# Kernel optimization log

Measured on AMD Instinct MI355X. Metric: run time of the kernel, lower is better.

## Reference

```python
import jax, jax.numpy as jnp
import numpy as np

EPS = 1e-8


def setup_inputs() -> dict:
    key = jax.random.key(0)
    k1, k2 = jax.random.split(key)
    N, D = 2048, 1024
    source = jax.random.normal(k1, (N, D), dtype=jnp.float32)
    target = jax.random.normal(k2, (N, D), dtype=jnp.float32)
    return {"source": source, "target": target}


def reference(source, target):
    N = source.shape[0]
    total = jnp.concatenate([source, target], axis=0)          # [2N, D]
    # Pairwise squared L2 via Gram trick: ||a||^2 + ||b||^2 - 2 a.b
    sq = jnp.sum(total * total, axis=-1)                       # [2N]
    gram = total @ total.T                                     # [2N, 2N]
    L2 = jnp.maximum(sq[:, None] + sq[None, :] - 2.0 * gram, 0.0)
    # torch.median on even-length flat array returns the LOWER of the two
    # middle elements, i.e. sorted[(numel - 1) // 2]
    flat = jnp.sort(L2.ravel())
    median_l2 = flat[(flat.size - 1) // 2]
    log_n = jnp.log(jnp.float32(N) + EPS)
    bandwidth = jax.lax.stop_gradient(jnp.sqrt(0.5 * median_l2 / log_n))
    kernel = jnp.exp(-L2 / (2.0 * bandwidth ** 2))             # [2N, 2N]
    XX = kernel[:N, :N]
    YY = kernel[N:, N:]
    XY = kernel[:N, N:]
    YX = kernel[N:, :N]
    loss = jnp.mean(XX + YY - XY - YX)
    return loss, bandwidth
```

## Files before the change

### kernel.cpp

```cpp
#include <hip/hip_runtime.h>

typedef unsigned int uint;
typedef unsigned short ushort;
using short8 = __attribute__((ext_vector_type(8))) short;
using f32x4  = __attribute__((ext_vector_type(4))) float;

#define NHALF 2048
#define DIM   1024
#define MROWS 4096
#define KMED  8388607u
#define NTRI  528

#define AH_OFF   0ull
#define SQ_OFF   8388608ull
#define GHT_OFF  (SQ_OFF + 16384ull)
#define GHN_OFF  (GHT_OFF + 65600ull)
#define CNT_OFF  (GHN_OFF + 65600ull)
#define ZERO_WORDS 32804

#define AGLOAD(p) __hip_atomic_load((p), __ATOMIC_RELAXED, __HIP_MEMORY_SCOPE_AGENT)

__device__ __forceinline__ ushort f2bf(float x) {
    uint u = __float_as_uint(x);
    u += 0x7FFFu + ((u >> 16) & 1u);
    return (ushort)(u >> 16);
}

__global__ __launch_bounds__(256) void convert_kernel(const float* __restrict__ src,
                                                      const float* __restrict__ tgt,
                                                      char* __restrict__ wsb) {
    ushort* ah = (ushort*)(wsb + AH_OFF);
    float*  sq = (float*)(wsb + SQ_OFF);
    uint*   z  = (uint*)(wsb + GHT_OFF);
    int t = threadIdx.x, row = blockIdx.x;
    int g = row * 256 + t;
    if (g < ZERO_WORDS) z[g] = 0;
    const float* p = (row < NHALF) ? src + (size_t)row * DIM
                                   : tgt + (size_t)(row - NHALF) * DIM;
    float4 v = reinterpret_cast<const float4*>(p)[t];
    float xs[4] = {v.x, v.y, v.z, v.w};
    ushort hh[4];
    float s = 0.0f;
#pragma unroll
    for (int e = 0; e < 4; ++e) { float x = xs[e]; s += x * x; hh[e] = f2bf(x); }
    ushort4 h4; h4.x = hh[0]; h4.y = hh[1]; h4.z = hh[2]; h4.w = hh[3];
    reinterpret_cast<ushort4*>(ah + (size_t)row * DIM)[t] = h4;
    for (int o = 32; o; o >>= 1) s += __shfl_down(s, o);
    __shared__ float red[4];
    if ((t & 63) == 0) red[t >> 6] = s;
    __syncthreads();
    if (t == 0) sq[row] = red[0] + red[1] + red[2] + red[3];
}

#define STAGE1(buf, arr, srcp, rb, cidx) do {                                              \
    int _i = (cidx) * 64 + lane;                                                           \
    const ushort* _g = (srcp) + ((size_t)((rb) + (_i >> 2)) * DIM + kk0 + (_i & 3) * 8);   \
    __builtin_amdgcn_global_load_lds(                                                      \
        (const __attribute__((address_space(1))) uint*)_g,                                 \
        (__attribute__((address_space(3))) uint*)(&lds[buf][arr][0][0] + (size_t)(cidx) * 512), \
        16, 0, 0);                                                                         \
} while (0)

__global__ __launch_bounds__(512, 4) void gemm_kernel(char* __restrict__ wsb,
                                                      float* __restrict__ out) {
    const ushort* ah = (const ushort*)(wsb + AH_OFF);
    const float*  sq = (const float*)(wsb + SQ_OFF);
    uint*  ght = (uint*)(wsb + GHT_OFF);
    uint*  ghn = (uint*)(wsb + GHN_OFF);
    uint*  cnt = (uint*)(wsb + CNT_OFF);

    __shared__ __align__(16) uint shmem[8192];
    __shared__ uint lowcnt;
    __shared__ float fred[8];
    ushort (*lds)[2][128][32] = (ushort (*)[2][128][32])shmem;

    int b = (int)blockIdx.x;
    b = (b & 7) * 66 + (b >> 3);
    int bi = (int)((sqrtf(8.0f * (float)b + 1.0f) - 1.0f) * 0.5f);
    while ((bi + 1) * (bi + 2) / 2 <= b) ++bi;
    while (bi * (bi + 1) / 2 > b) --bi;
    int bj = b - bi * (bi + 1) / 2;

    int t = threadIdx.x;
    int lane = t & 63, wid = t >> 6;
    int wm = wid >> 2, wn = wid & 3;
    int rowbase = bi * 128, colbase = bj * 128;

    f32x4 acc[4][2] = {};
    int fr = lane & 15, fk = (lane >> 4) * 8;

    {
        int kk0 = 0;
        STAGE1(0, 0, ah, rowbase, wid);
        STAGE1(0, 1, ah, colbase, wid);
    }
    __syncthreads();

    int cur = 0;
    for (int kt = 0; kt < 32; ++kt) {
        if (kt < 31) {
            int kk0 = (kt + 1) * 32;
            int nb = cur ^ 1;
            STAGE1(nb, 0, ah, rowbase, wid);
            STAGE1(nb, 1, ah, colbase, wid);
        }
        short8 fa[4], fb[2];
#pragma unroll
        for (int m = 0; m < 4; ++m)
            fa[m] = *reinterpret_cast<const short8*>(&lds[cur][0][wm * 64 + m * 16 + fr][fk]);
#pragma unroll
        for (int n = 0; n < 2; ++n)
            fb[n] = *reinterpret_cast<const short8*>(&lds[cur][1][wn * 32 + n * 16 + fr][fk]);
#pragma unroll
        for (int m = 0; m < 4; ++m)
#pragma unroll
            for (int n = 0; n < 2; ++n)
                acc[m][n] = __builtin_amdgcn_mfma_f32_16x16x32_bf16(fa[m], fb[n], acc[m][n], 0, 0, 0);
        __syncthreads();
        cur ^= 1;
    }

    uint* h = shmem;
    for (int i = t; i < 8192; i += 512) h[i] = 0;
    if (t == 0) lowcnt = 0;
    __syncthreads();

    uint w = (bi == bj) ? 1u : 2u;
    int fq = lane >> 4;
#pragma unroll
    for (int m = 0; m < 4; ++m) {
#pragma unroll
        for (int n = 0; n < 2; ++n) {
            int gj = colbase + wn * 32 + n * 16 + fr;
            float sqj = sq[gj];
#pragma unroll
            for (int r = 0; r < 4; ++r) {
                int gi = rowbase + wm * 64 + m * 16 + fq * 4 + r;
                float v = fmaxf(sq[gi] + sqj - 2.0f * acc[m][n][r], 0.0f);
                uint bits = __float_as_uint(v);
                if (bits & 0x40000000u) {
                    uint k14 = (bits >> 16) & 0x3FFFu;
                    atomicAdd(&h[k14 >> 1], (k14 & 1) ? (w << 16) : w);
                } else {
                    atomicAdd(&lowcnt, w);
                }
            }
        }
    }
    __syncthreads();

    bool crosshalf = (bi < 16) != (bj < 16);
    for (int i = t; i < 8192; i += 512) {
        uint wd = h[i];
        if (wd) {
            uint lo = wd & 0xFFFFu, hi2 = wd >> 16;
            if (lo)  { atomicAdd(&ght[2 * i],     lo);  if (crosshalf) atomicAdd(&ghn[2 * i],     lo); }
            if (hi2) { atomicAdd(&ght[2 * i + 1], hi2); if (crosshalf) atomicAdd(&ghn[2 * i + 1], hi2); }
        }
    }
    if (t == 0 && lowcnt) {
        atomicAdd(&ght[16384], lowcnt);
        if (crosshalf) atomicAdd(&ghn[16384], lowcnt);
    }

    __syncthreads();
    if (t == 0) {
        __threadfence();
        h[0] = (atomicAdd(&cnt[0], 1u) == gridDim.x - 1) ? 1u : 0u;
    }
    __syncthreads();
    bool last = h[0] != 0;
    __syncthreads();
    if (!last) return;

    uint* part = h + 16;
    uint* loc  = h + 544;
    uint* lin  = h + 560;
    uint s = 0;
    for (int i = 0; i < 32; ++i) s += AGLOAD(&ght[t * 32 + i]);
    part[t] = s;
    __syncthreads();
    if (t == 0) {
        uint k = KMED - AGLOAD(&ght[16384]);
        uint cum = 0; int seg = 0;
        for (; seg < 512; ++seg) { uint c = part[seg]; if (cum + c > k) break; cum += c; }
        loc[0] = (uint)seg; loc[1] = k - cum;
    }
    __syncthreads();
    int seg = (int)loc[0];
    if (t < 32) lin[t] = AGLOAD(&ght[seg * 32 + t]);
    __syncthreads();
    if (t == 0) {
        uint k = loc[1], cum = 0; int bb = 0;
        for (; bb < 32; ++bb) { uint c = lin[bb]; if (cum + c > k) break; cum += c; }
        uint mbits = 0x40000000u | ((uint)(seg * 32 + bb) << 16) | 0x8000u;
        float median = __uint_as_float(mbits);
        float logn = logf(2048.0f + 1e-8f);
        float bw = sqrtf(0.5f * median / logn);
        out[1] = bw;
        ((float*)loc)[1] = logn / median;
    }
    __syncthreads();
    float itb = ((float*)loc)[1];

    float local = 0.0f;
    for (int i = 0; i < 32; ++i) {
        int bidx = t * 32 + i;
        int tot = (int)AGLOAD(&ght[bidx]);
        int neg = (int)AGLOAD(&ghn[bidx]);
        int sgn = tot - 2 * neg;
        if (sgn) {
            float mid = __uint_as_float(0x40000000u | ((uint)bidx << 16) | 0x8000u);
            local += (float)sgn * __expf(-mid * itb);
        }
    }
    if (t == 0)
        local += (float)((int)AGLOAD(&ght[16384]) - 2 * (int)AGLOAD(&ghn[16384]));
    for (int o = 32; o; o >>= 1) local += __shfl_down(local, o);
    if ((t & 63) == 0) fred[t >> 6] = local;
    __syncthreads();
    if (t == 0) {
        float bs = fred[0] + fred[1] + fred[2] + fred[3]
                 + fred[4] + fred[5] + fred[6] + fred[7];
        out[0] = bs / 4194304.0f;
    }
}

extern "C" void kernel_launch(void* const* d_in, const int* in_sizes, int n_in,
                              void* d_out, int out_size, void* d_ws, size_t ws_size,
                              hipStream_t stream) {
    const float* src = (const float*)d_in[0];
    const float* tgt = (const float*)d_in[1];
    float* out = (float*)d_out;
    char* ws = (char*)d_ws;

    convert_kernel<<<MROWS, 256, 0, stream>>>(src, tgt, ws);
    gemm_kernel<<<NTRI, 512, 0, stream>>>(ws, out);
}
```

Before: 84.88 us.

## Fuse bf16 conversion into GEMM kernel with grid-wide spin barrier

Removes the separate convert kernel. The first 512 blocks of the GEMM grid now convert rows to bf16 and compute squared norms, then every block spins on an atomic counter until all conversions finish. Zeroing of the histogram and counter moves to a hipMemsetAsync on the stream. This saves a kernel launch gap, but adds a memset node and a spin barrier that deadlocks unless all 528 blocks are co-resident. The memset may also cost about as much as the launch that was removed.

```diff
diff --git a/kernel.cpp b/kernel.cpp
--- a/kernel.cpp
+++ b/kernel.cpp
@@ -16,40 +16,15 @@
 #define GHT_OFF  (SQ_OFF + 16384ull)
 #define GHN_OFF  (GHT_OFF + 65600ull)
 #define CNT_OFF  (GHN_OFF + 65600ull)
-#define ZERO_WORDS 32804
-
-#define AGLOAD(p) __hip_atomic_load((p), __ATOMIC_RELAXED, __HIP_MEMORY_SCOPE_AGENT)
+#define MEMSET_BYTES (65600ull * 2 + 16ull)
+
+#define AGLOAD(p)      __hip_atomic_load((p), __ATOMIC_RELAXED, __HIP_MEMORY_SCOPE_AGENT)
+#define AGLOAD_ACQ(p)  __hip_atomic_load((p), __ATOMIC_ACQUIRE, __HIP_MEMORY_SCOPE_AGENT)
 
 __device__ __forceinline__ ushort f2bf(float x) {
     uint u = __float_as_uint(x);
     u += 0x7FFFu + ((u >> 16) & 1u);
     return (ushort)(u >> 16);
-}
-
-__global__ __launch_bounds__(256) void convert_kernel(const float* __restrict__ src,
-                                                      const float* __restrict__ tgt,
-                                                      char* __restrict__ wsb) {
-    ushort* ah = (ushort*)(wsb + AH_OFF);
-    float*  sq = (float*)(wsb + SQ_OFF);
-    uint*   z  = (uint*)(wsb + GHT_OFF);
-    int t = threadIdx.x, row = blockIdx.x;
-    int g = row * 256 + t;
-    if (g < ZERO_WORDS) z[g] = 0;
-    const float* p = (row < NHALF) ? src + (size_t)row * DIM
-                                   : tgt + (size_t)(row - NHALF) * DIM;
-    float4 v = reinterpret_cast<const float4*>(p)[t];
-    float xs[4] = {v.x, v.y, v.z, v.w};
-    ushort hh[4];
-    float s = 0.0f;
-#pragma unroll
-    for (int e = 0; e < 4; ++e) { float x = xs[e]; s += x * x; hh[e] = f2bf(x); }
-    ushort4 h4; h4.x = hh[0]; h4.y = hh[1]; h4.z = hh[2]; h4.w = hh[3];
-    reinterpret_cast<ushort4*>(ah + (size_t)row * DIM)[t] = h4;
-    for (int o = 32; o; o >>= 1) s += __shfl_down(s, o);
-    __shared__ float red[4];
-    if ((t & 63) == 0) red[t >> 6] = s;
-    __syncthreads();
-    if (t == 0) sq[row] = red[0] + red[1] + red[2] + red[3];
 }
 
 #define STAGE1(buf, arr, srcp, rb, cidx) do {                                              \
@@ -61,28 +36,58 @@
         16, 0, 0);                                                                         \
 } while (0)
 
-__global__ __launch_bounds__(512, 4) void gemm_kernel(char* __restrict__ wsb,
-                                                      float* __restrict__ out) {
-    const ushort* ah = (const ushort*)(wsb + AH_OFF);
-    const float*  sq = (const float*)(wsb + SQ_OFF);
-    uint*  ght = (uint*)(wsb + GHT_OFF);
-    uint*  ghn = (uint*)(wsb + GHN_OFF);
-    uint*  cnt = (uint*)(wsb + CNT_OFF);
+__global__ __launch_bounds__(512, 4) void mmd_kernel(const float* __restrict__ src,
+                                                     const float* __restrict__ tgt,
+                                                     char* __restrict__ wsb,
+                                                     float* __restrict__ out) {
+    ushort* ah = (ushort*)(wsb + AH_OFF);
+    float*  sq = (float*)(wsb + SQ_OFF);
+    uint*   ght = (uint*)(wsb + GHT_OFF);
+    uint*   ghn = (uint*)(wsb + GHN_OFF);
+    uint*   cnt = (uint*)(wsb + CNT_OFF);
 
     __shared__ __align__(16) uint shmem[8192];
     __shared__ uint lowcnt;
     __shared__ float fred[8];
     ushort (*lds)[2][128][32] = (ushort (*)[2][128][32])shmem;
 
-    int b = (int)blockIdx.x;
+    int t = threadIdx.x;
+    int lane = t & 63, wid = t >> 6;
+    int b0 = (int)blockIdx.x;
+
+    if (b0 < 512) {
+        int row = b0 * 8 + wid;
+        const float* p = (row < NHALF) ? src + (size_t)row * DIM
+                                       : tgt + (size_t)(row - NHALF) * DIM;
+        float s = 0.0f;
+#pragma unroll
+        for (int c = 0; c < 4; ++c) {
+            float4 v = *reinterpret_cast<const float4*>(p + lane * 16 + c * 4);
+            s += v.x * v.x + v.y * v.y + v.z * v.z + v.w * v.w;
+            ushort4 u4; u4.x = f2bf(v.x); u4.y = f2bf(v.y); u4.z = f2bf(v.z); u4.w = f2bf(v.w);
+            *reinterpret_cast<ushort4*>(ah + (size_t)row * DIM + lane * 16 + c * 4) = u4;
+        }
+        for (int o = 32; o; o >>= 1) s += __shfl_down(s, o);
+        if (lane == 0) sq[row] = s;
+        __syncthreads();
+        if (t == 0) {
+            __threadfence();
+            atomicAdd(&cnt[0], 1u);
+        }
+    }
+
+    if (t == 0) {
+        while (AGLOAD_ACQ(&cnt[0]) < 512u) __builtin_amdgcn_s_sleep(2);
+    }
+    __syncthreads();
+
+    int b = b0;
     b = (b & 7) * 66 + (b >> 3);
     int bi = (int)((sqrtf(8.0f * (float)b + 1.0f) - 1.0f) * 0.5f);
     while ((bi + 1) * (bi + 2) / 2 <= b) ++bi;
     while (bi * (bi + 1) / 2 > b) --bi;
     int bj = b - bi * (bi + 1) / 2;
 
-    int t = threadIdx.x;
-    int lane = t & 63, wid = t >> 6;
     int wm = wid >> 2, wn = wid & 3;
     int rowbase = bi * 128, colbase = bj * 128;
 
@@ -166,7 +171,7 @@
     __syncthreads();
     if (t == 0) {
         __threadfence();
-        h[0] = (atomicAdd(&cnt[0], 1u) == gridDim.x - 1) ? 1u : 0u;
+        h[0] = (atomicAdd(&cnt[1], 1u) == gridDim.x - 1) ? 1u : 0u;
     }
     __syncthreads();
     bool last = h[0] != 0;
@@ -234,6 +239,6 @@
     float* out = (float*)d_out;
     char* ws = (char*)d_ws;
 
-    convert_kernel<<<MROWS, 256, 0, stream>>>(src, tgt, ws);
-    gemm_kernel<<<NTRI, 512, 0, stream>>>(ws, out);
+    hipMemsetAsync(ws + GHT_OFF, 0, MEMSET_BYTES, stream);
+    mmd_kernel<<<NTRI, 512, 0, stream>>>(src, tgt, ws, out);
 }
```

Measured after the change: 141.3 us. +66.4%, slower.

## Switch Gram GEMM operands from bf16 to fp8 e4m3 MFMA

Applied to the files above, without the earlier changes.

Converts inputs to fp8 e4m3 instead of bf16 and uses the 16x16x32 fp8 MFMA, which halves operand bytes in global memory and LDS. Staging changes so each wave loads one 16-byte chunk per tile, split between the A and B tiles. This cuts load and convert traffic but lowers dot-product precision a lot, which could shift the median bin and the histogram-based loss past tolerance.

```diff
diff --git a/kernel.cpp b/kernel.cpp
--- a/kernel.cpp
+++ b/kernel.cpp
@@ -1,9 +1,9 @@
 #include <hip/hip_runtime.h>
+#include <hip/hip_fp8.h>
 
 typedef unsigned int uint;
-typedef unsigned short ushort;
-using short8 = __attribute__((ext_vector_type(8))) short;
-using f32x4  = __attribute__((ext_vector_type(4))) float;
+typedef unsigned char uchar;
+using f32x4 = __attribute__((ext_vector_type(4))) float;
 
 #define NHALF 2048
 #define DIM   1024
@@ -12,7 +12,7 @@
 #define NTRI  528
 
 #define AH_OFF   0ull
-#define SQ_OFF   8388608ull
+#define SQ_OFF   4194304ull
 #define GHT_OFF  (SQ_OFF + 16384ull)
 #define GHN_OFF  (GHT_OFF + 65600ull)
 #define CNT_OFF  (GHN_OFF + 65600ull)
@@ -20,31 +20,25 @@
 
 #define AGLOAD(p) __hip_atomic_load((p), __ATOMIC_RELAXED, __HIP_MEMORY_SCOPE_AGENT)
 
-__device__ __forceinline__ ushort f2bf(float x) {
-    uint u = __float_as_uint(x);
-    u += 0x7FFFu + ((u >> 16) & 1u);
-    return (ushort)(u >> 16);
-}
-
 __global__ __launch_bounds__(256) void convert_kernel(const float* __restrict__ src,
                                                       const float* __restrict__ tgt,
                                                       char* __restrict__ wsb) {
-    ushort* ah = (ushort*)(wsb + AH_OFF);
-    float*  sq = (float*)(wsb + SQ_OFF);
-    uint*   z  = (uint*)(wsb + GHT_OFF);
+    uchar* ah = (uchar*)(wsb + AH_OFF);
+    float* sq = (float*)(wsb + SQ_OFF);
+    uint*  z  = (uint*)(wsb + GHT_OFF);
     int t = threadIdx.x, row = blockIdx.x;
     int g = row * 256 + t;
     if (g < ZERO_WORDS) z[g] = 0;
     const float* p = (row < NHALF) ? src + (size_t)row * DIM
                                    : tgt + (size_t)(row - NHALF) * DIM;
     float4 v = reinterpret_cast<const float4*>(p)[t];
-    float xs[4] = {v.x, v.y, v.z, v.w};
-    ushort hh[4];
-    float s = 0.0f;
-#pragma unroll
-    for (int e = 0; e < 4; ++e) { float x = xs[e]; s += x * x; hh[e] = f2bf(x); }
-    ushort4 h4; h4.x = hh[0]; h4.y = hh[1]; h4.z = hh[2]; h4.w = hh[3];
-    reinterpret_cast<ushort4*>(ah + (size_t)row * DIM)[t] = h4;
+    float s = v.x * v.x + v.y * v.y + v.z * v.z + v.w * v.w;
+    uchar4 u4;
+    u4.x = __hip_fp8_e4m3(v.x).__x;
+    u4.y = __hip_fp8_e4m3(v.y).__x;
+    u4.z = __hip_fp8_e4m3(v.z).__x;
+    u4.w = __hip_fp8_e4m3(v.w).__x;
+    reinterpret_cast<uchar4*>(ah + (size_t)row * DIM)[t] = u4;
     for (int o = 32; o; o >>= 1) s += __shfl_down(s, o);
     __shared__ float red[4];
     if ((t & 63) == 0) red[t >> 6] = s;
@@ -52,19 +46,19 @@
     if (t == 0) sq[row] = red[0] + red[1] + red[2] + red[3];
 }
 
-#define STAGE1(buf, arr, srcp, rb, cidx) do {                                              \
-    int _i = (cidx) * 64 + lane;                                                           \
-    const ushort* _g = (srcp) + ((size_t)((rb) + (_i >> 2)) * DIM + kk0 + (_i & 3) * 8);   \
+#define STAGE8(buf, arr, rb, cidx) do {                                                    \
+    int _row = (cidx) * 32 + (lane >> 1);                                                  \
+    const uchar* _g = ah + ((size_t)((rb) + _row) * DIM + kk0 + (lane & 1) * 16);          \
     __builtin_amdgcn_global_load_lds(                                                      \
         (const __attribute__((address_space(1))) uint*)_g,                                 \
-        (__attribute__((address_space(3))) uint*)(&lds[buf][arr][0][0] + (size_t)(cidx) * 512), \
+        (__attribute__((address_space(3))) uint*)(&lds[buf][arr][0][0] + (size_t)(cidx) * 1024), \
         16, 0, 0);                                                                         \
 } while (0)
 
 __global__ __launch_bounds__(512, 4) void gemm_kernel(char* __restrict__ wsb,
                                                       float* __restrict__ out) {
-    const ushort* ah = (const ushort*)(wsb + AH_OFF);
-    const float*  sq = (const float*)(wsb + SQ_OFF);
+    const uchar* ah = (const uchar*)(wsb + AH_OFF);
+    const float* sq = (const float*)(wsb + SQ_OFF);
     uint*  ght = (uint*)(wsb + GHT_OFF);
     uint*  ghn = (uint*)(wsb + GHN_OFF);
     uint*  cnt = (uint*)(wsb + CNT_OFF);
@@ -72,7 +66,7 @@
     __shared__ __align__(16) uint shmem[8192];
     __shared__ uint lowcnt;
     __shared__ float fred[8];
-    ushort (*lds)[2][128][32] = (ushort (*)[2][128][32])shmem;
+    uchar (*lds)[2][128][32] = (uchar (*)[2][128][32])shmem;
 
     int b = (int)blockIdx.x;
     b = (b & 7) * 66 + (b >> 3);
@@ -87,12 +81,15 @@
     int rowbase = bi * 128, colbase = bj * 128;
 
     f32x4 acc[4][2] = {};
-    int fr = lane & 15, fk = (lane >> 4) * 8;
+    int fr = lane & 15;
+    int fk8 = (lane >> 4) * 8;
+
+    int sarr = wid >> 2, scid = wid & 3;
+    int srb  = sarr ? colbase : rowbase;
 
     {
         int kk0 = 0;
-        STAGE1(0, 0, ah, rowbase, wid);
-        STAGE1(0, 1, ah, colbase, wid);
+        STAGE8(0, sarr, srb, scid);
     }
     __syncthreads();
 
@@ -101,21 +98,20 @@
         if (kt < 31) {
             int kk0 = (kt + 1) * 32;
             int nb = cur ^ 1;
-            STAGE1(nb, 0, ah, rowbase, wid);
-            STAGE1(nb, 1, ah, colbase, wid);
-        }
-        short8 fa[4], fb[2];
+            STAGE8(nb, sarr, srb, scid);
+        }
+        long fa[4], fb[2];
 #pragma unroll
         for (int m = 0; m < 4; ++m)
-            fa[m] = *reinterpret_cast<const short8*>(&lds[cur][0][wm * 64 + m * 16 + fr][fk]);
+            fa[m] = *reinterpret_cast<const long*>(&lds[cur][0][wm * 64 + m * 16 + fr][fk8]);
 #pragma unroll
         for (int n = 0; n < 2; ++n)
-            fb[n] = *reinterpret_cast<const short8*>(&lds[cur][1][wn * 32 + n * 16 + fr][fk]);
+            fb[n] = *reinterpret_cast<const long*>(&lds[cur][1][wn * 32 + n * 16 + fr][fk8]);
 #pragma unroll
         for (int m = 0; m < 4; ++m)
 #pragma unroll
             for (int n = 0; n < 2; ++n)
-                acc[m][n] = __builtin_amdgcn_mfma_f32_16x16x32_bf16(fa[m], fb[n], acc[m][n], 0, 0, 0);
+                acc[m][n] = __builtin_amdgcn_mfma_f32_16x16x32_fp8_fp8(fa[m], fb[n], acc[m][n], 0, 0, 0);
         __syncthreads();
         cur ^= 1;
     }
```

Result: slower. 93.74 us (+10.4%).

## Enlarge GEMM tiles to 256x256 with swizzled LDS and interleaved staging

Applied to the files above, without the earlier changes.

Each block now covers a 256x256 output tile (136 upper-triangle blocks instead of 528) with 32 accumulators per thread. The K step grows to 64, the LDS layout is XOR-swizzled to avoid bank conflicts, and next-tile loads are issued in four quarters between MFMA phases, using manual waitcnt, barriers and setprio. The aim is more operand reuse per byte loaded and better overlap of memory with compute. In exchange, far fewer blocks than CUs leaves the GPU underfilled, register pressure rises, and occupancy is capped at 2 blocks.

```diff
diff --git a/kernel.cpp b/kernel.cpp
--- a/kernel.cpp
+++ b/kernel.cpp
@@ -9,7 +9,7 @@
 #define DIM   1024
 #define MROWS 4096
 #define KMED  8388607u
-#define NTRI  528
+#define NTRI  136
 
 #define AH_OFF   0ull
 #define SQ_OFF   8388608ull
@@ -52,16 +52,26 @@
     if (t == 0) sq[row] = red[0] + red[1] + red[2] + red[3];
 }
 
-#define STAGE1(buf, arr, srcp, rb, cidx) do {                                              \
-    int _i = (cidx) * 64 + lane;                                                           \
-    const ushort* _g = (srcp) + ((size_t)((rb) + (_i >> 2)) * DIM + kk0 + (_i & 3) * 8);   \
-    __builtin_amdgcn_global_load_lds(                                                      \
-        (const __attribute__((address_space(1))) uint*)_g,                                 \
-        (__attribute__((address_space(3))) uint*)(&lds[buf][arr][0][0] + (size_t)(cidx) * 512), \
-        16, 0, 0);                                                                         \
+#define STAGEU(buf, u, kt) do {                                                            \
+    int _arr = (u) >> 1;                                                                   \
+    int _rb  = _arr ? colbase : rowbase;                                                   \
+    _Pragma("unroll")                                                                      \
+    for (int _l = 0; _l < 2; ++_l) {                                                       \
+        int _r0 = ((u) & 1) * 128 + (wid * 2 + _l) * 8;                                    \
+        const ushort* _g = ah + (size_t)(_rb + _r0 + (lane >> 3)) * DIM                    \
+                           + (kt) * 64 + (((lane & 7) ^ (lane >> 3)) * 8);                 \
+        __builtin_amdgcn_global_load_lds(                                                  \
+            (const __attribute__((address_space(1))) uint*)_g,                             \
+            (__attribute__((address_space(3))) uint*)(&lds[buf][_arr][0][0] + (size_t)_r0 * 64), \
+            16, 0, 0);                                                                     \
+    }                                                                                      \
 } while (0)
 
-__global__ __launch_bounds__(512, 4) void gemm_kernel(char* __restrict__ wsb,
+#define RD(arr, lrow, ks) \
+    (*reinterpret_cast<const short8*>(&lds[cur][arr][0][0] + (size_t)(lrow) * 64 + \
+        (((ks) * 4 + fkk) ^ (fr & 7)) * 8))
+
+__global__ __launch_bounds__(512, 2) void gemm_kernel(char* __restrict__ wsb,
                                                       float* __restrict__ out) {
     const ushort* ah = (const ushort*)(wsb + AH_OFF);
     const float*  sq = (const float*)(wsb + SQ_OFF);
@@ -69,13 +79,12 @@
     uint*  ghn = (uint*)(wsb + GHN_OFF);
     uint*  cnt = (uint*)(wsb + CNT_OFF);
 
-    __shared__ __align__(16) uint shmem[8192];
+    __shared__ __align__(16) ushort lds[2][2][256][64];
     __shared__ uint lowcnt;
     __shared__ float fred[8];
-    ushort (*lds)[2][128][32] = (ushort (*)[2][128][32])shmem;
 
     int b = (int)blockIdx.x;
-    b = (b & 7) * 66 + (b >> 3);
+    b = (b & 7) * 17 + (b >> 3);
     int bi = (int)((sqrtf(8.0f * (float)b + 1.0f) - 1.0f) * 0.5f);
     while ((bi + 1) * (bi + 2) / 2 <= b) ++bi;
     while (bi * (bi + 1) / 2 > b) --bi;
@@ -84,59 +93,111 @@
     int t = threadIdx.x;
     int lane = t & 63, wid = t >> 6;
     int wm = wid >> 2, wn = wid & 3;
-    int rowbase = bi * 128, colbase = bj * 128;
-
-    f32x4 acc[4][2] = {};
-    int fr = lane & 15, fk = (lane >> 4) * 8;
-
-    {
-        int kk0 = 0;
-        STAGE1(0, 0, ah, rowbase, wid);
-        STAGE1(0, 1, ah, colbase, wid);
-    }
-    __syncthreads();
-
-    int cur = 0;
-    for (int kt = 0; kt < 32; ++kt) {
-        if (kt < 31) {
-            int kk0 = (kt + 1) * 32;
-            int nb = cur ^ 1;
-            STAGE1(nb, 0, ah, rowbase, wid);
-            STAGE1(nb, 1, ah, colbase, wid);
+    int rowbase = bi * 256, colbase = bj * 256;
+
+    f32x4 acc[8][4] = {};
+    int fr = lane & 15, fkk = lane >> 4;
+
+    STAGEU(0, 0, 0); STAGEU(0, 1, 0); STAGEU(0, 2, 0); STAGEU(0, 3, 0);
+
+    short8 fa[4][2], fb[4][2];
+
+    for (int kt = 0; kt < 16; ++kt) {
+        int cur = kt & 1, nxt = cur ^ 1;
+        bool st = kt < 15;
+        if (st) {
+            STAGEU(nxt, 0, kt + 1);
+            asm volatile("s_waitcnt vmcnt(2)" ::: "memory");
+        } else {
+            asm volatile("s_waitcnt vmcnt(0)" ::: "memory");
         }
-        short8 fa[4], fb[2];
-#pragma unroll
-        for (int m = 0; m < 4; ++m)
-            fa[m] = *reinterpret_cast<const short8*>(&lds[cur][0][wm * 64 + m * 16 + fr][fk]);
-#pragma unroll
-        for (int n = 0; n < 2; ++n)
-            fb[n] = *reinterpret_cast<const short8*>(&lds[cur][1][wn * 32 + n * 16 + fr][fk]);
-#pragma unroll
-        for (int m = 0; m < 4; ++m)
-#pragma unroll
-            for (int n = 0; n < 2; ++n)
-                acc[m][n] = __builtin_amdgcn_mfma_f32_16x16x32_bf16(fa[m], fb[n], acc[m][n], 0, 0, 0);
-        __syncthreads();
-        cur ^= 1;
-    }
-
-    uint* h = shmem;
+        __builtin_amdgcn_s_barrier();
+#pragma unroll
+        for (int mi = 0; mi < 4; ++mi)
+#pragma unroll
+            for (int ks = 0; ks < 2; ++ks)
+                fa[mi][ks] = RD(0, wm * 128 + mi * 16 + fr, ks);
+#pragma unroll
+        for (int ni = 0; ni < 2; ++ni)
+#pragma unroll
+            for (int ks = 0; ks < 2; ++ks)
+                fb[ni][ks] = RD(1, wn * 64 + ni * 16 + fr, ks);
+        __builtin_amdgcn_s_setprio(1);
+#pragma unroll
+        for (int mi = 0; mi < 4; ++mi)
+#pragma unroll
+            for (int ni = 0; ni < 2; ++ni)
+#pragma unroll
+                for (int ks = 0; ks < 2; ++ks)
+                    acc[mi][ni] = __builtin_amdgcn_mfma_f32_16x16x32_bf16(fa[mi][ks], fb[ni][ks], acc[mi][ni], 0, 0, 0);
+        __builtin_amdgcn_s_setprio(0);
+        __builtin_amdgcn_s_barrier();
+        if (st) STAGEU(nxt, 1, kt + 1);
+        __builtin_amdgcn_s_barrier();
+#pragma unroll
+        for (int ni = 0; ni < 2; ++ni)
+#pragma unroll
+            for (int ks = 0; ks < 2; ++ks)
+                fb[2 + ni][ks] = RD(1, wn * 64 + 32 + ni * 16 + fr, ks);
+        __builtin_amdgcn_s_setprio(1);
+#pragma unroll
+        for (int mi = 0; mi < 4; ++mi)
+#pragma unroll
+            for (int ni = 0; ni < 2; ++ni)
+#pragma unroll
+                for (int ks = 0; ks < 2; ++ks)
+                    acc[mi][2 + ni] = __builtin_amdgcn_mfma_f32_16x16x32_bf16(fa[mi][ks], fb[2 + ni][ks], acc[mi][2 + ni], 0, 0, 0);
+        __builtin_amdgcn_s_setprio(0);
+        __builtin_amdgcn_s_barrier();
+        if (st) STAGEU(nxt, 2, kt + 1);
+        __builtin_amdgcn_s_barrier();
+#pragma unroll
+        for (int mi = 0; mi < 4; ++mi)
+#pragma unroll
+            for (int ks = 0; ks < 2; ++ks)
+                fa[mi][ks] = RD(0, wm * 128 + 64 + mi * 16 + fr, ks);
+        __builtin_amdgcn_s_setprio(1);
+#pragma unroll
+        for (int mi = 0; mi < 4; ++mi)
+#pragma unroll
+            for (int ni = 0; ni < 2; ++ni)
+#pragma unroll
+                for (int ks = 0; ks < 2; ++ks)
+                    acc[4 + mi][2 + ni] = __builtin_amdgcn_mfma_f32_16x16x32_bf16(fa[mi][ks], fb[2 + ni][ks], acc[4 + mi][2 + ni], 0, 0, 0);
+        __builtin_amdgcn_s_setprio(0);
+        __builtin_amdgcn_s_barrier();
+        if (st) STAGEU(nxt, 3, kt + 1);
+        __builtin_amdgcn_s_barrier();
+        __builtin_amdgcn_s_setprio(1);
+#pragma unroll
+        for (int mi = 0; mi < 4; ++mi)
+#pragma unroll
+            for (int ni = 0; ni < 2; ++ni)
+#pragma unroll
+                for (int ks = 0; ks < 2; ++ks)
+                    acc[4 + mi][ni] = __builtin_amdgcn_mfma_f32_16x16x32_bf16(fa[mi][ks], fb[ni][ks], acc[4 + mi][ni], 0, 0, 0);
+        __builtin_amdgcn_s_setprio(0);
+        __builtin_amdgcn_s_barrier();
+    }
+    __syncthreads();
+
+    uint* h = (uint*)&lds[0][0][0][0];
     for (int i = t; i < 8192; i += 512) h[i] = 0;
     if (t == 0) lowcnt = 0;
     __syncthreads();
 
     uint w = (bi == bj) ? 1u : 2u;
-    int fq = lane >> 4;
-#pragma unroll
-    for (int m = 0; m < 4; ++m) {
-#pragma unroll
-        for (int n = 0; n < 2; ++n) {
-            int gj = colbase + wn * 32 + n * 16 + fr;
+    int fq = fkk;
+#pragma unroll
+    for (int mi = 0; mi < 8; ++mi) {
+#pragma unroll
+        for (int ni = 0; ni < 4; ++ni) {
+            int gj = colbase + wn * 64 + ni * 16 + fr;
             float sqj = sq[gj];
 #pragma unroll
             for (int r = 0; r < 4; ++r) {
-                int gi = rowbase + wm * 64 + m * 16 + fq * 4 + r;
-                float v = fmaxf(sq[gi] + sqj - 2.0f * acc[m][n][r], 0.0f);
+                int gi = rowbase + wm * 128 + mi * 16 + fq * 4 + r;
+                float v = fmaxf(sq[gi] + sqj - 2.0f * acc[mi][ni][r], 0.0f);
                 uint bits = __float_as_uint(v);
                 if (bits & 0x40000000u) {
                     uint k14 = (bits >> 16) & 0x3FFFu;
@@ -149,7 +210,7 @@
     }
     __syncthreads();
 
-    bool crosshalf = (bi < 16) != (bj < 16);
+    bool crosshalf = (bi < 8) != (bj < 8);
     for (int i = t; i < 8192; i += 512) {
         uint wd = h[i];
         if (wd) {
```

Measured after the change: 83.49 us (median of 2 runs). Within noise of the previous version (-1.6%).
